# Optimization experiments

Measured on AMD Instinct MI355X. Metric: run time of the kernel, lower is better.

## Reference

```python
import jax, jax.numpy as jnp
import numpy as np

B, S, D_IN, D_H = 8, 2048, 512, 512

def setup_inputs() -> dict:
    key = jax.random.key(0)
    ks = jax.random.split(key, 7)
    s = 1.0 / np.sqrt(D_IN)
    return {
        "x": jax.random.normal(ks[0], (B, S, D_IN), dtype=jnp.float32),
        "Wq": jax.random.uniform(ks[1], (D_H, D_IN), jnp.float32, -s, s),
        "bq": jax.random.uniform(ks[2], (D_H,), jnp.float32, -s, s),
        "Wk": jax.random.uniform(ks[3], (D_H, D_IN), jnp.float32, -s, s),
        "bk": jax.random.uniform(ks[4], (D_H,), jnp.float32, -s, s),
        "Wv": jax.random.uniform(ks[5], (D_H, D_IN), jnp.float32, -s, s),
        "bv": jax.random.uniform(ks[6], (D_H,), jnp.float32, -s, s),
    }

def reference(x, Wq, bq, Wk, bk, Wv, bv):
    # torch Linear: y = x @ W.T + b
    Q = jnp.einsum('bsd,hd->bsh', x, Wq) + bq
    K = jnp.einsum('bsd,hd->bsh', x, Wk) + bk
    V = jnp.einsum('bsd,hd->bsh', x, Wv) + bv
    scale = jnp.sqrt(jnp.asarray(D_H, dtype=x.dtype))
    scores = jnp.einsum('bqh,bkh->bqk', Q, K) / scale  # [B,S,S]
    attn = jax.nn.softmax(scores, axis=-1)
    return jnp.einsum('bqk,bkh->bqh', attn, V)
```

## Files before the change

### kernel.cpp

```cpp
#include <hip/hip_runtime.h>
#include <hip/hip_bf16.h>
#include <cstdint>

#define B_   8
#define S_   2048
#define DIN  512
#define DH   512

typedef __attribute__((ext_vector_type(8))) short  short8;
typedef __attribute__((ext_vector_type(4))) short  short4_;
typedef __attribute__((ext_vector_type(4))) float  float4_;

__device__ inline unsigned short f2bf(float f) {
    union { float f; unsigned u; } v; v.f = f;
    unsigned u = v.u;
    u += 0x7fffu + ((u >> 16) & 1u);
    return (unsigned short)(u >> 16);
}

__device__ inline void gload_lds16(const void* g, void* l) {
    __builtin_amdgcn_global_load_lds(
        (const __attribute__((address_space(1))) void*)g,
        (__attribute__((address_space(3))) void*)l, 16, 0, 0);
}

template <int C>
__device__ inline float fdpp(float x) {
    return __int_as_float(__builtin_amdgcn_update_dpp(0, __float_as_int(x), C, 0xF, 0xF, true));
}
__device__ inline float rsum16(float v) {
    v += fdpp<0x140>(v);
    v += fdpp<0x141>(v);
    v += fdpp<27>(v);
    v += fdpp<177>(v);
    return v;
}

__global__ __launch_bounds__(256) void conv_bf16(
    const float* __restrict__ x,
    const float* __restrict__ Wq, const float* __restrict__ Wk, const float* __restrict__ Wv,
    unsigned short* __restrict__ xb, unsigned short* __restrict__ wb)
{
    const int NX4 = (B_ * S_ * DIN) / 4;
    const int NW4 = (DH * DIN) / 4;
    const int total = NX4 + 3 * NW4;
    for (int i = blockIdx.x * blockDim.x + threadIdx.x; i < total;
         i += gridDim.x * blockDim.x) {
        const float4_* src; unsigned short* dst; int j;
        if (i < NX4)             { src = (const float4_*)x;  dst = xb;            j = i; }
        else if (i < NX4 + NW4)  { src = (const float4_*)Wq; dst = wb;            j = i - NX4; }
        else if (i < NX4 + 2*NW4){ src = (const float4_*)Wk; dst = wb + DH*DIN;   j = i - NX4 - NW4; }
        else                     { src = (const float4_*)Wv; dst = wb + 2*DH*DIN; j = i - NX4 - 2*NW4; }
        float4_ v = src[j];
        short4_ o;
        o[0] = (short)f2bf(v[0]); o[1] = (short)f2bf(v[1]);
        o[2] = (short)f2bf(v[2]); o[3] = (short)f2bf(v[3]);
        ((short4_*)dst)[j] = o;
    }
}

__global__ __launch_bounds__(256) void qkv_gemm(
    const unsigned short* __restrict__ xb,
    const unsigned short* __restrict__ wb,
    const float* __restrict__ bq, const float* __restrict__ bk, const float* __restrict__ bv,
    unsigned short* __restrict__ qws, unsigned short* __restrict__ kws,
    unsigned short* __restrict__ vt2)
{
    __shared__ __align__(16) unsigned short smem[17408];

    const int tm   = blockIdx.x;
    const int tc   = blockIdx.y;
    const int mat  = tc >> 2;
    const int nb   = (tc & 3) * 128;
    const int tid  = threadIdx.x;
    const int w    = tid >> 6;
    const int lane = tid & 63;
    const int l15  = lane & 15;
    const int quad = lane >> 4;
    const int wm   = (w & 1) * 64;
    const int wn   = (w >> 1) * 64;
    const int m0   = tm * 128;

    const unsigned short* wmat = wb + (size_t)mat * DH * DIN;

    float4_ zero = {0.f, 0.f, 0.f, 0.f};
    float4_ acc[4][4];
    #pragma unroll
    for (int i = 0; i < 4; i++)
        #pragma unroll
        for (int j = 0; j < 4; j++) acc[i][j] = zero;

    const int lr = lane >> 2;
    const int lb = (lane & 3) * 16;

    auto stage = [&](int kk, int bufi) {
        unsigned short* Ab = smem + bufi * 8192;
        unsigned short* Bb = smem + 4096 + bufi * 8192;
        #pragma unroll
        for (int c = 0; c < 2; c++) {
            int r = w * 32 + c * 16;
            const unsigned char* gA = (const unsigned char*)(xb + (size_t)(m0 + r) * DIN + kk);
            gload_lds16(gA + (size_t)lr * (DIN * 2) + lb, (void*)(Ab + r * 32));
            const unsigned char* gB = (const unsigned char*)(wmat + (size_t)(nb + r) * DIN + kk);
            gload_lds16(gB + (size_t)lr * (DIN * 2) + lb, (void*)(Bb + r * 32));
        }
    };

    stage(0, 0);
    for (int ki = 0; ki < 16; ki++) {
        __syncthreads();
        if (ki < 15) stage((ki + 1) * 32, (ki + 1) & 1);
        const unsigned short* Ab = smem + (ki & 1) * 8192;
        const unsigned short* Bb = smem + 4096 + (ki & 1) * 8192;
        short8 af[4], bf[4];
        #pragma unroll
        for (int mt = 0; mt < 4; mt++)
            af[mt] = *(const short8*)(Ab + (wm + mt * 16 + l15) * 32 + quad * 8);
        #pragma unroll
        for (int nt = 0; nt < 4; nt++)
            bf[nt] = *(const short8*)(Bb + (wn + nt * 16 + l15) * 32 + quad * 8);
        #pragma unroll
        for (int mt = 0; mt < 4; mt++)
            #pragma unroll
            for (int nt = 0; nt < 4; nt++)
                acc[mt][nt] = __builtin_amdgcn_mfma_f32_16x16x32_bf16(af[mt], bf[nt], acc[mt][nt], 0, 0, 0);
    }

    if (mat < 2) {
        const float* bias  = (mat == 0) ? bq : bk;
        const float  scale = (mat == 0) ? 0.06375870430742225f : 1.0f;
        unsigned short* dst = (mat == 0) ? qws : kws;
        #pragma unroll
        for (int nt = 0; nt < 4; nt++) {
            int n = nb + wn + nt * 16 + l15;
            float bv_ = bias[n];
            #pragma unroll
            for (int mt = 0; mt < 4; mt++) {
                #pragma unroll
                for (int r = 0; r < 4; r++) {
                    int m = m0 + wm + mt * 16 + quad * 4 + r;
                    dst[(size_t)m * DH + n] = f2bf((acc[mt][nt][r] + bv_) * scale);
                }
            }
        }
    } else {
        __syncthreads();
        unsigned short* trans = smem;
        #pragma unroll
        for (int nt = 0; nt < 4; nt++) {
            int dloc = wn + nt * 16 + l15;
            float bv_ = bv[nb + dloc];
            #pragma unroll
            for (int mt = 0; mt < 4; mt++) {
                short4_ pk;
                #pragma unroll
                for (int r = 0; r < 4; r++) pk[r] = (short)f2bf(acc[mt][nt][r] + bv_);
                *(short4_*)(trans + dloc * 136 + wm + mt * 16 + quad * 4) = pk;
            }
        }
        __syncthreads();
        int dl   = tid >> 1;
        int h    = tid & 1;
        int dh_g = nb + dl;
        int bi   = m0 >> 11;
        int tile0 = (m0 & 2047) >> 4;
        unsigned char* vt2b = (unsigned char*)vt2;
        #pragma unroll
        for (int t = 0; t < 4; t++) {
            int tl = h * 4 + t;
            const uint4* c = (const uint4*)(trans + dl * 136 + tl * 16);
            unsigned char* dst = vt2b + ((size_t)(bi * 128 + tile0 + tl) << 14) + dh_g * 32;
            ((uint4*)dst)[0] = c[0];
            ((uint4*)dst)[1] = c[1];
        }
    }
}

__global__ __launch_bounds__(512, 2) void attn(
    const unsigned short* __restrict__ qws,
    const unsigned short* __restrict__ kws,
    const unsigned short* __restrict__ vt2,
    float* __restrict__ out)
{
    __shared__ __align__(16) unsigned char smem[76288];

    const int bid  = blockIdx.x;
    const int b    = bid & 7;
    const int qt_b = bid >> 3;
    const int tid  = threadIdx.x;
    const int w    = tid >> 6;
    const int g    = w >> 2;
    const int wl   = w & 3;
    const int lane = tid & 63;
    const int l15  = lane & 15;
    const int quad = lane >> 4;

    const int qrow0  = b * S_ + qt_b * 64;
    const int myqrow = qrow0 + wl * 16;

    const unsigned short* kgrp = kws + (size_t)(b * S_ + g * 1024) * DH;
    const unsigned char*  vtb  = (const unsigned char*)vt2;

    unsigned char* kb    = smem + g * 32768;
    unsigned char* pbase = smem + 65536 + g * 5120;
    float*         lbuf  = (float*)(smem + 75776);

    short8 qf[16];
    {
        const short8* qp = (const short8*)(qws + (size_t)(myqrow + l15) * DH);
        #pragma unroll
        for (int ksi = 0; ksi < 16; ksi++) qf[ksi] = qp[ksi * 4 + quad];
    }

    float4_ zero = {0.f, 0.f, 0.f, 0.f};
    float4_ o[32];
    #pragma unroll
    for (int i = 0; i < 32; i++) o[i] = zero;
    float l_[4] = {0.f, 0.f, 0.f, 0.f};

    short4_ vreg[8];

    auto stageK = [&](int n, int bufi) {
        #pragma unroll
        for (int i = 0; i < 4; i++) {
            int row = wl * 4 + i;
            const unsigned char* gp =
                (const unsigned char*)(kgrp + (size_t)(n * 16 + row) * DH);
            gload_lds16(gp + ((lane ^ (row & 7)) << 4),
                        kb + bufi * 16384 + row * 1024);
        }
    };

    auto loadV = [&](int n) {
        const unsigned char* base = vtb + ((size_t)(b * 128 + g * 64 + n) << 14)
                                  + (size_t)(wl * 128 + l15) * 32 + quad * 8;
        #pragma unroll
        for (int dht = 0; dht < 8; dht++)
            vreg[dht] = *(const short4_*)(base + dht * 512);
    };

    auto doPV = [&](int bufi) {
        const unsigned char* pp = pbase + bufi * 2560;
        short4_ pa[4];
        #pragma unroll
        for (int qt = 0; qt < 4; qt++)
            pa[qt] = *(const short4_*)(pp + (qt * 16 + l15) * 40 + quad * 8);
        __builtin_amdgcn_s_setprio(1);
        #pragma unroll
        for (int dht = 0; dht < 8; dht++)
            #pragma unroll
            for (int qt = 0; qt < 4; qt++)
                o[qt * 8 + dht] = __builtin_amdgcn_mfma_f32_16x16x16bf16_1k(pa[qt], vreg[dht], o[qt * 8 + dht], 0, 0, 0);
        __builtin_amdgcn_s_setprio(0);
    };

    stageK(0, 0);

    for (int it = 0; it < 64; it++) {
        __syncthreads();

        if (it) loadV(it - 1);
        if (it < 63) stageK(it + 1, (it + 1) & 1);

        const unsigned char* kt_ = kb + (it & 1) * 16384;
        float4_ s0 = zero, s1 = zero;
        __builtin_amdgcn_s_setprio(1);
        #pragma unroll
        for (int ksi = 0; ksi < 16; ksi += 2) {
            short8 k0 = *(const short8*)(kt_ + l15 * 1024 + ((( ksi      * 4 + quad) ^ (l15 & 7)) << 4));
            short8 k1 = *(const short8*)(kt_ + l15 * 1024 + ((((ksi + 1) * 4 + quad) ^ (l15 & 7)) << 4));
            s0 = __builtin_amdgcn_mfma_f32_16x16x32_bf16(qf[ksi],     k0, s0, 0, 0, 0);
            s1 = __builtin_amdgcn_mfma_f32_16x16x32_bf16(qf[ksi + 1], k1, s1, 0, 0, 0);
        }
        __builtin_amdgcn_s_setprio(0);
        float4_ sc = s0 + s1;

        unsigned short* pp = (unsigned short*)(pbase + (it & 1) * 2560);
        #pragma unroll
        for (int r = 0; r < 4; r++) {
            float p = __builtin_exp2f(sc[r]);
            l_[r] += p;
            pp[(wl * 16 + quad * 4 + r) * 20 + l15] = f2bf(p);
        }

        if (it) doPV((it - 1) & 1);
    }

    __syncthreads();
    loadV(63);
    doPV(1);

    float lsum[4];
    #pragma unroll
    for (int r = 0; r < 4; r++) lsum[r] = rsum16(l_[r]);
    if (l15 == 0) {
        #pragma unroll
        for (int r = 0; r < 4; r++)
            lbuf[g * 64 + wl * 16 + quad * 4 + r] = lsum[r];
    }

    float* om = (float*)(smem + (wl & 1) * 33280);
    #pragma unroll
    for (int p = 0; p < 2; p++) {
        __syncthreads();
        if (g == 1 && (wl >> 1) == p) {
            #pragma unroll
            for (int qt = 0; qt < 4; qt++)
                #pragma unroll
                for (int dht = 0; dht < 8; dht++)
                    #pragma unroll
                    for (int r = 0; r < 4; r++)
                        om[(qt * 16 + quad * 4 + r) * 130 + dht * 16 + l15] = o[qt * 8 + dht][r];
        }
        __syncthreads();
        if (g == 0 && (wl >> 1) == p) {
            #pragma unroll
            for (int qt = 0; qt < 4; qt++) {
                float rl[4];
                #pragma unroll
                for (int r = 0; r < 4; r++) {
                    int row = qt * 16 + quad * 4 + r;
                    rl[r] = 1.f / (lbuf[row] + lbuf[64 + row]);
                }
                #pragma unroll
                for (int dht = 0; dht < 8; dht++)
                    #pragma unroll
                    for (int r = 0; r < 4; r++) {
                        int row = qt * 16 + quad * 4 + r;
                        out[(size_t)(qrow0 + row) * DH + wl * 128 + dht * 16 + l15] =
                            (o[qt * 8 + dht][r] + om[row * 130 + dht * 16 + l15]) * rl[r];
                    }
            }
        }
    }
}

extern "C" void kernel_launch(void* const* d_in, const int* in_sizes, int n_in,
                              void* d_out, int out_size, void* d_ws, size_t ws_size,
                              hipStream_t stream) {
    const float* x  = (const float*)d_in[0];
    const float* Wq = (const float*)d_in[1];
    const float* bq = (const float*)d_in[2];
    const float* Wk = (const float*)d_in[3];
    const float* bk = (const float*)d_in[4];
    const float* Wv = (const float*)d_in[5];
    const float* bv = (const float*)d_in[6];
    float* out = (float*)d_out;

    unsigned short* qws = (unsigned short*)d_ws;
    unsigned short* kws = qws + (size_t)B_ * S_ * DH;
    unsigned short* vt2 = kws + (size_t)B_ * S_ * DH;

    unsigned short* xb = (unsigned short*)d_out;
    unsigned short* wb = xb + (size_t)B_ * S_ * DIN;

    conv_bf16<<<dim3(2048), dim3(256), 0, stream>>>(x, Wq, Wk, Wv, xb, wb);
    qkv_gemm<<<dim3(128, 12), dim3(256), 0, stream>>>(xb, wb, bq, bk, bv, qws, kws, vt2);
    attn<<<dim3(256), dim3(512), 0, stream>>>(qws, kws, vt2, out);
}
```

Before: 289.2 us.

## Stage V through LDS and split PV output columns across all waves

V tiles are now copied into double-buffered LDS with async global-to-LDS loads instead of being read straight into registers. In the PV step each wave reads P and V from both key groups and computes a 64-column slice of the output with the wider 16x16x32 MFMA. This removes the final cross-group reduction through LDS and halves the output accumulator registers. The cost is that LDS use grows to about 139 KB per block, which likely allows only one 512-thread block per CU instead of the two the launch bounds ask for; the s_setprio hints are also dropped.

```diff
diff --git a/kernel.cpp b/kernel.cpp
--- a/kernel.cpp
+++ b/kernel.cpp
@@ -182,7 +182,7 @@
     const unsigned short* __restrict__ vt2,
     float* __restrict__ out)
 {
-    __shared__ __align__(16) unsigned char smem[76288];
+    __shared__ __align__(16) unsigned char smem[141824];
 
     const int bid  = blockIdx.x;
     const int b    = bid & 7;
@@ -201,9 +201,10 @@
     const unsigned short* kgrp = kws + (size_t)(b * S_ + g * 1024) * DH;
     const unsigned char*  vtb  = (const unsigned char*)vt2;
 
-    unsigned char* kb    = smem + g * 32768;
-    unsigned char* pbase = smem + 65536 + g * 5120;
-    float*         lbuf  = (float*)(smem + 75776);
+    unsigned char* kb    = smem + g * 65536;
+    unsigned char* vb    = smem + g * 65536 + 32768;
+    unsigned char* pbase = smem + 131072 + g * 5120;
+    float*         lbuf  = (float*)(smem + 141312);
 
     short8 qf[16];
     {
@@ -213,12 +214,10 @@
     }
 
     float4_ zero = {0.f, 0.f, 0.f, 0.f};
-    float4_ o[32];
+    float4_ o[16];
     #pragma unroll
-    for (int i = 0; i < 32; i++) o[i] = zero;
+    for (int i = 0; i < 16; i++) o[i] = zero;
     float l_[4] = {0.f, 0.f, 0.f, 0.f};
-
-    short4_ vreg[8];
 
     auto stageK = [&](int n, int bufi) {
         #pragma unroll
@@ -230,28 +229,31 @@
                         kb + bufi * 16384 + row * 1024);
         }
     };
-
-    auto loadV = [&](int n) {
-        const unsigned char* base = vtb + ((size_t)(b * 128 + g * 64 + n) << 14)
-                                  + (size_t)(wl * 128 + l15) * 32 + quad * 8;
-        #pragma unroll
-        for (int dht = 0; dht < 8; dht++)
-            vreg[dht] = *(const short4_*)(base + dht * 512);
+    auto stageV = [&](int n, int bufi) {
+        const unsigned char* base =
+            vtb + ((size_t)(b * 128 + g * 64 + n) << 14) + wl * 4096;
+        #pragma unroll
+        for (int i = 0; i < 4; i++)
+            gload_lds16(base + i * 1024 + lane * 16,
+                        vb + bufi * 16384 + wl * 4096 + i * 1024);
     };
 
     auto doPV = [&](int bufi) {
-        const unsigned char* pp = pbase + bufi * 2560;
-        short4_ pa[4];
+        const unsigned char* pq = smem + 131072 + (quad >> 1) * 5120
+                                + bufi * 2560 + (quad & 1) * 16;
+        const unsigned char* vq = smem + (quad >> 1) * 65536 + 32768
+                                + bufi * 16384 + (quad & 1) * 16;
+        short8 pa[4];
         #pragma unroll
         for (int qt = 0; qt < 4; qt++)
-            pa[qt] = *(const short4_*)(pp + (qt * 16 + l15) * 40 + quad * 8);
-        __builtin_amdgcn_s_setprio(1);
-        #pragma unroll
-        for (int dht = 0; dht < 8; dht++)
+            pa[qt] = *(const short8*)(pq + (qt * 16 + l15) * 40);
+        #pragma unroll
+        for (int dht = 0; dht < 4; dht++) {
+            short8 vf = *(const short8*)(vq + (size_t)(w * 64 + dht * 16 + l15) * 32);
             #pragma unroll
             for (int qt = 0; qt < 4; qt++)
-                o[qt * 8 + dht] = __builtin_amdgcn_mfma_f32_16x16x16bf16_1k(pa[qt], vreg[dht], o[qt * 8 + dht], 0, 0, 0);
-        __builtin_amdgcn_s_setprio(0);
+                o[qt * 4 + dht] = __builtin_amdgcn_mfma_f32_16x16x32_bf16(pa[qt], vf, o[qt * 4 + dht], 0, 0, 0);
+        }
     };
 
     stageK(0, 0);
@@ -259,12 +261,11 @@
     for (int it = 0; it < 64; it++) {
         __syncthreads();
 
-        if (it) loadV(it - 1);
         if (it < 63) stageK(it + 1, (it + 1) & 1);
+        stageV(it, it & 1);
 
         const unsigned char* kt_ = kb + (it & 1) * 16384;
         float4_ s0 = zero, s1 = zero;
-        __builtin_amdgcn_s_setprio(1);
         #pragma unroll
         for (int ksi = 0; ksi < 16; ksi += 2) {
             short8 k0 = *(const short8*)(kt_ + l15 * 1024 + ((( ksi      * 4 + quad) ^ (l15 & 7)) << 4));
@@ -272,7 +273,6 @@
             s0 = __builtin_amdgcn_mfma_f32_16x16x32_bf16(qf[ksi],     k0, s0, 0, 0, 0);
             s1 = __builtin_amdgcn_mfma_f32_16x16x32_bf16(qf[ksi + 1], k1, s1, 0, 0, 0);
         }
-        __builtin_amdgcn_s_setprio(0);
         float4_ sc = s0 + s1;
 
         unsigned short* pp = (unsigned short*)(pbase + (it & 1) * 2560);
@@ -287,7 +287,6 @@
     }
 
     __syncthreads();
-    loadV(63);
     doPV(1);
 
     float lsum[4];
@@ -298,40 +297,24 @@
         for (int r = 0; r < 4; r++)
             lbuf[g * 64 + wl * 16 + quad * 4 + r] = lsum[r];
     }
-
-    float* om = (float*)(smem + (wl & 1) * 33280);
+    __syncthreads();
+
     #pragma unroll
-    for (int p = 0; p < 2; p++) {
-        __syncthreads();
-        if (g == 1 && (wl >> 1) == p) {
-            #pragma unroll
-            for (int qt = 0; qt < 4; qt++)
-                #pragma unroll
-                for (int dht = 0; dht < 8; dht++)
-                    #pragma unroll
-                    for (int r = 0; r < 4; r++)
-                        om[(qt * 16 + quad * 4 + r) * 130 + dht * 16 + l15] = o[qt * 8 + dht][r];
-        }
-        __syncthreads();
-        if (g == 0 && (wl >> 1) == p) {
-            #pragma unroll
-            for (int qt = 0; qt < 4; qt++) {
-                float rl[4];
-                #pragma unroll
-                for (int r = 0; r < 4; r++) {
-                    int row = qt * 16 + quad * 4 + r;
-                    rl[r] = 1.f / (lbuf[row] + lbuf[64 + row]);
-                }
-                #pragma unroll
-                for (int dht = 0; dht < 8; dht++)
-                    #pragma unroll
-                    for (int r = 0; r < 4; r++) {
-                        int row = qt * 16 + quad * 4 + r;
-                        out[(size_t)(qrow0 + row) * DH + wl * 128 + dht * 16 + l15] =
-                            (o[qt * 8 + dht][r] + om[row * 130 + dht * 16 + l15]) * rl[r];
-                    }
+    for (int qt = 0; qt < 4; qt++) {
+        float rl[4];
+        #pragma unroll
+        for (int r = 0; r < 4; r++) {
+            int row = qt * 16 + quad * 4 + r;
+            rl[r] = 1.f / (lbuf[row] + lbuf[64 + row]);
+        }
+        #pragma unroll
+        for (int dht = 0; dht < 4; dht++)
+            #pragma unroll
+            for (int r = 0; r < 4; r++) {
+                int row = qt * 16 + quad * 4 + r;
+                out[(size_t)(qrow0 + row) * DH + w * 64 + dht * 16 + l15] =
+                    o[qt * 4 + dht][r] * rl[r];
             }
-        }
     }
 }
 
```

Result: faster. 262.5 us (-9.2%).
